# Kernel tuning notes

Measured on AMD Instinct MI355X. Metric: run time of the kernel, lower is better.

The kernel has to match this reference:

```python
import jax, jax.numpy as jnp
import numpy as np

N, H, S = 2048, 512, 256

def setup_inputs() -> dict:
    key = jax.random.key(0)
    k1, k2, k3 = jax.random.split(key, 3)
    hidden_states = jax.random.normal(k1, (N, H, S), dtype=jnp.float32)
    # xavier_uniform-ish scale for W and context vector
    limW = float(np.sqrt(6.0 / (H + H)))
    attention_weights = jax.random.uniform(k2, (H, H), dtype=jnp.float32, minval=-limW, maxval=limW)
    attention_bias = jnp.zeros((H, 1), dtype=jnp.float32)
    limc = float(np.sqrt(6.0 / (H + 1)))
    context_vector = jax.random.uniform(k3, (H, 1), dtype=jnp.float32, minval=-limc, maxval=limc)
    return {
        "hidden_states": hidden_states,
        "attention_weights": attention_weights,
        "attention_bias": attention_bias,
        "context_vector": context_vector,
    }

def reference(hidden_states, attention_weights, attention_bias, context_vector):
    # hidden_states: (N, H, S)
    hs_t = jnp.swapaxes(hidden_states, 1, 2)              # (N, S, H)
    score = jnp.tanh(hs_t @ attention_weights + attention_bias[:, 0])  # (N, S, H)
    alignment = (score @ context_vector)[..., 0]          # (N, S)
    attn = jax.nn.softmax(alignment, axis=1)              # (N, S)
    context = jnp.einsum('ns,nhs->nh', attn, hidden_states)  # (N, H)
    return context
```

## Files before the change

kernel.cpp:

```cpp
#include <hip/hip_runtime.h>
#include <hip/hip_bf16.h>
#include <stdint.h>
#include <stddef.h>

typedef __attribute__((ext_vector_type(8))) short short8;
typedef __attribute__((ext_vector_type(4))) short short4v;
typedef __attribute__((ext_vector_type(4))) float f32x4;
typedef __attribute__((ext_vector_type(16))) float f32x16;

#define NB 2048
#define HD 512
#define SD 256

#define AS_STR 24
#define WS_STR 24

__device__ __forceinline__ short f2bf(float x) {
  __hip_bfloat16 h = __float2bfloat16(x);
  return *reinterpret_cast<short*>(&h);
}

__device__ __forceinline__ float fast_tanh(float x) {
  x = fminf(fmaxf(x, -15.f), 15.f);
  float e = __expf(2.f * x);
  return __fdividef(e - 1.f, e + 1.f);
}

__global__ __launch_bounds__(256) void wconv_kernel(const float* __restrict__ W,
                                                    short* __restrict__ Wtb16) {
  __shared__ float tile[32][33];
  const int bx = blockIdx.x;
  const int tk0 = (bx & 15) * 32;
  const int tj0 = (bx >> 4) * 32;
  const int lx = threadIdx.x & 31;
  const int ly = threadIdx.x >> 5;
  for (int r = 0; r < 4; ++r) {
    int yy = ly + r * 8;
    tile[yy][lx] = W[(size_t)(tk0 + yy) * HD + tj0 + lx];
  }
  __syncthreads();
  for (int r = 0; r < 4; ++r) {
    int yy = ly + r * 8;
    const int k = tk0 + lx;
    Wtb16[(size_t)(k >> 4) * (HD * 16) + (size_t)(tj0 + yy) * 16 + (k & 15)] =
        f2bf(tile[lx][yy]);
  }
}

__global__ void __launch_bounds__(512, 4)
align_kernel(const float* __restrict__ hs, const short* __restrict__ Wtb16,
             const float* __restrict__ bias, const float* __restrict__ ctxv,
             float* __restrict__ align_out)
{
  __shared__ short As[2][64 * AS_STR];
  __shared__ short Ws[2][512 * WS_STR];
  __shared__ float abuf[64];

  const int tid = threadIdx.x;
  const int n = blockIdx.x >> 2;
  const int s0 = (blockIdx.x & 3) * 64;
  const float* hsn = hs + (size_t)n * (HD * SD) + s0;

  if (tid < 64) abuf[tid] = 0.f;

  const int a_s = tid & 63;
  const int a_kq = (tid >> 6) & 3;
  const int w_j = tid;

  if (tid < 256) {
    const float* src = hsn + (size_t)(a_kq * 4) * SD + a_s;
    short4v pk;
    pk[0] = f2bf(src[0]); pk[1] = f2bf(src[SD]);
    pk[2] = f2bf(src[2 * SD]); pk[3] = f2bf(src[3 * SD]);
    *(short4v*)&As[0][a_s * AS_STR + a_kq * 4] = pk;
  }
  {
    const short* wsrc = Wtb16 + (size_t)w_j * 16;
    *(short8*)&Ws[0][w_j * WS_STR] = *(const short8*)wsrc;
    *(short8*)&Ws[0][w_j * WS_STR + 8] = *(const short8*)(wsrc + 8);
  }
  __syncthreads();

  const int lane = tid & 63;
  const int wid = tid >> 6;
  const int jb = wid * 64;
  const int l31 = lane & 31;
  const int hg = lane >> 5;

  f32x16 acc[2][2];
  #pragma unroll
  for (int i = 0; i < 2; ++i)
    #pragma unroll
    for (int p = 0; p < 2; ++p)
      #pragma unroll
      for (int q = 0; q < 16; ++q) acc[i][p][q] = 0.f;

  const int afo = l31 * AS_STR + hg * 8;
  const int wfo = (jb + l31) * WS_STR + hg * 8;

  for (int kt = 0; kt < 32; ++kt) {
    const int cur = kt & 1;

    float av[4];
    short8 wv0, wv1;
    if (kt < 31) {
      if (tid < 256) {
        const float* src = hsn + (size_t)((kt + 1) * 16 + a_kq * 4) * SD + a_s;
        #pragma unroll
        for (int e = 0; e < 4; ++e) av[e] = src[(size_t)e * SD];
      }
      const short* wsrc = Wtb16 + (size_t)(kt + 1) * (HD * 16) + (size_t)w_j * 16;
      wv0 = *(const short8*)wsrc;
      wv1 = *(const short8*)(wsrc + 8);
    }

    short8 wf0 = *(const short8*)&Ws[cur][wfo];
    short8 wf1 = *(const short8*)&Ws[cur][wfo + 32 * WS_STR];
    short8 af0 = *(const short8*)&As[cur][afo];
    short8 af1 = *(const short8*)&As[cur][afo + 32 * AS_STR];

    __builtin_amdgcn_s_setprio(1);
    acc[0][0] = __builtin_amdgcn_mfma_f32_32x32x16_bf16(wf0, af0, acc[0][0], 0, 0, 0);
    acc[0][1] = __builtin_amdgcn_mfma_f32_32x32x16_bf16(wf1, af0, acc[0][1], 0, 0, 0);
    acc[1][0] = __builtin_amdgcn_mfma_f32_32x32x16_bf16(wf0, af1, acc[1][0], 0, 0, 0);
    acc[1][1] = __builtin_amdgcn_mfma_f32_32x32x16_bf16(wf1, af1, acc[1][1], 0, 0, 0);
    __builtin_amdgcn_s_setprio(0);

    if (kt < 31) {
      const int nxt = cur ^ 1;
      if (tid < 256) {
        short4v pk;
        #pragma unroll
        for (int e = 0; e < 4; ++e) pk[e] = f2bf(av[e]);
        *(short4v*)&As[nxt][a_s * AS_STR + a_kq * 4] = pk;
      }
      *(short8*)&Ws[nxt][w_j * WS_STR] = wv0;
      *(short8*)&Ws[nxt][w_j * WS_STR + 8] = wv1;
    }
    __syncthreads();
  }

  float part0 = 0.f, part1 = 0.f;
  #pragma unroll
  for (int p = 0; p < 2; ++p) {
    const int jfr = jb + p * 32 + hg * 4;
    #pragma unroll
    for (int g = 0; g < 4; ++g) {
      const int j4 = jfr + g * 8;
      f32x4 bv = *(const f32x4*)(bias + j4);
      f32x4 cv = *(const f32x4*)(ctxv + j4);
      #pragma unroll
      for (int r = 0; r < 4; ++r) {
        const int q = g * 4 + r;
        part0 += fast_tanh(acc[0][p][q] + bv[r]) * cv[r];
        part1 += fast_tanh(acc[1][p][q] + bv[r]) * cv[r];
      }
    }
  }
  part0 += __shfl_xor(part0, 32);
  part1 += __shfl_xor(part1, 32);
  if (lane < 32) {
    atomicAdd(&abuf[l31], part0);
    atomicAdd(&abuf[32 + l31], part1);
  }
  __syncthreads();
  if (tid < 64) align_out[(size_t)n * SD + s0 + tid] = abuf[tid];
}

__global__ __launch_bounds__(256) void ctx_kernel(const float* __restrict__ hs,
                                                  const float* __restrict__ align_in,
                                                  float* __restrict__ out)
{
  __shared__ __align__(16) float attn_s[256];
  __shared__ float red[8];
  const int n = blockIdx.x;
  const int t = threadIdx.x;
  const int lane = t & 63, wid = t >> 6;

  float a = align_in[(size_t)n * 256 + t];
  float m = a;
  #pragma unroll
  for (int off = 32; off; off >>= 1) m = fmaxf(m, __shfl_xor(m, off));
  if (lane == 0) red[wid] = m;
  __syncthreads();
  m = fmaxf(fmaxf(red[0], red[1]), fmaxf(red[2], red[3]));
  float e = __expf(a - m);
  float s = e;
  #pragma unroll
  for (int off = 32; off; off >>= 1) s += __shfl_xor(s, off);
  if (lane == 0) red[4 + wid] = s;
  __syncthreads();
  s = red[4] + red[5] + red[6] + red[7];
  attn_s[t] = e / s;
  __syncthreads();

  const int grp = t & 7;
  const int hrow = t >> 3;
  float av[32];
  #pragma unroll
  for (int u = 0; u < 8; ++u) {
    float4 v = *(const float4*)&attn_s[grp * 32 + u * 4];
    av[4*u+0] = v.x; av[4*u+1] = v.y; av[4*u+2] = v.z; av[4*u+3] = v.w;
  }
  const float* hb = hs + (size_t)n * (HD * SD) + grp * 32;
  for (int it = 0; it < 16; ++it) {
    const int h = it * 32 + hrow;
    const float4* p = (const float4*)(hb + (size_t)h * SD);
    float acc = 0.f;
    #pragma unroll
    for (int u = 0; u < 8; ++u) {
      float4 v = p[u];
      acc += av[4*u+0]*v.x + av[4*u+1]*v.y + av[4*u+2]*v.z + av[4*u+3]*v.w;
    }
    acc += __shfl_xor(acc, 1);
    acc += __shfl_xor(acc, 2);
    acc += __shfl_xor(acc, 4);
    if (grp == 0) out[(size_t)n * HD + h] = acc;
  }
}

extern "C" void kernel_launch(void* const* d_in, const int* in_sizes, int n_in,
                              void* d_out, int out_size, void* d_ws, size_t ws_size,
                              hipStream_t stream) {
  (void)in_sizes; (void)n_in; (void)out_size; (void)ws_size;
  const float* hs = (const float*)d_in[0];
  const float* W  = (const float*)d_in[1];
  const float* b  = (const float*)d_in[2];
  const float* c  = (const float*)d_in[3];
  float* out = (float*)d_out;

  float* align_ws = (float*)d_ws;
  short* Wtb16 = (short*)((char*)d_ws + (size_t)NB * SD * 4);

  wconv_kernel<<<256, 256, 0, stream>>>(W, Wtb16);
  align_kernel<<<NB * 4, 512, 0, stream>>>(hs, Wtb16, b, c, align_ws);
  ctx_kernel<<<NB, 256, 0, stream>>>(hs, align_ws, out);
}
```

Baseline: 806.3 us.

## Stage full activation tile once in LDS and stream W fragments from global

New measurement: 714.2 us. 1.13x faster.

```diff
diff --git a/kernel.cpp b/kernel.cpp
--- a/kernel.cpp
+++ b/kernel.cpp
@@ -4,7 +4,6 @@
 #include <stddef.h>
 
 typedef __attribute__((ext_vector_type(8))) short short8;
-typedef __attribute__((ext_vector_type(4))) short short4v;
 typedef __attribute__((ext_vector_type(4))) float f32x4;
 typedef __attribute__((ext_vector_type(16))) float f32x16;
 
@@ -12,8 +11,7 @@
 #define HD 512
 #define SD 256
 
-#define AS_STR 24
-#define WS_STR 24
+#define AROW 516
 
 __device__ __forceinline__ short f2bf(float x) {
   __hip_bfloat16 h = __float2bfloat16(x);
@@ -52,8 +50,7 @@
              const float* __restrict__ bias, const float* __restrict__ ctxv,
              float* __restrict__ align_out)
 {
-  __shared__ short As[2][64 * AS_STR];
-  __shared__ short Ws[2][512 * WS_STR];
+  __shared__ short As[64 * AROW];
   __shared__ float abuf[64];
 
   const int tid = threadIdx.x;
@@ -63,21 +60,18 @@
 
   if (tid < 64) abuf[tid] = 0.f;
 
-  const int a_s = tid & 63;
-  const int a_kq = (tid >> 6) & 3;
-  const int w_j = tid;
-
-  if (tid < 256) {
-    const float* src = hsn + (size_t)(a_kq * 4) * SD + a_s;
-    short4v pk;
-    pk[0] = f2bf(src[0]); pk[1] = f2bf(src[SD]);
-    pk[2] = f2bf(src[2 * SD]); pk[3] = f2bf(src[3 * SD]);
-    *(short4v*)&As[0][a_s * AS_STR + a_kq * 4] = pk;
-  }
   {
-    const short* wsrc = Wtb16 + (size_t)w_j * 16;
-    *(short8*)&Ws[0][w_j * WS_STR] = *(const short8*)wsrc;
-    *(short8*)&Ws[0][w_j * WS_STR + 8] = *(const short8*)(wsrc + 8);
+    const int a_s = tid & 63;
+    const int a_kg = tid >> 6;
+    #pragma unroll
+    for (int o = 0; o < 8; ++o) {
+      const int k0 = a_kg * 64 + o * 8;
+      const float* src = hsn + (size_t)k0 * SD + a_s;
+      short8 pk;
+      #pragma unroll
+      for (int e = 0; e < 8; ++e) pk[e] = f2bf(src[(size_t)e * SD]);
+      *(short8*)&As[a_s * AROW + k0] = pk;
+    }
   }
   __syncthreads();
 
@@ -95,29 +89,16 @@
       #pragma unroll
       for (int q = 0; q < 16; ++q) acc[i][p][q] = 0.f;
 
-  const int afo = l31 * AS_STR + hg * 8;
-  const int wfo = (jb + l31) * WS_STR + hg * 8;
-
-  for (int kt = 0; kt < 32; ++kt) {
-    const int cur = kt & 1;
-
-    float av[4];
-    short8 wv0, wv1;
-    if (kt < 31) {
-      if (tid < 256) {
-        const float* src = hsn + (size_t)((kt + 1) * 16 + a_kq * 4) * SD + a_s;
-        #pragma unroll
-        for (int e = 0; e < 4; ++e) av[e] = src[(size_t)e * SD];
-      }
-      const short* wsrc = Wtb16 + (size_t)(kt + 1) * (HD * 16) + (size_t)w_j * 16;
-      wv0 = *(const short8*)wsrc;
-      wv1 = *(const short8*)(wsrc + 8);
-    }
-
-    short8 wf0 = *(const short8*)&Ws[cur][wfo];
-    short8 wf1 = *(const short8*)&Ws[cur][wfo + 32 * WS_STR];
-    short8 af0 = *(const short8*)&As[cur][afo];
-    short8 af1 = *(const short8*)&As[cur][afo + 32 * AS_STR];
+  const short* wlane = Wtb16 + (size_t)(jb + l31) * 16 + hg * 8;
+  const int afo = l31 * AROW + hg * 8;
+
+  #pragma unroll 4
+  for (int kb = 0; kb < 32; ++kb) {
+    const short* wk = wlane + (size_t)kb * (HD * 16);
+    short8 wf0 = *(const short8*)(wk);
+    short8 wf1 = *(const short8*)(wk + 32 * 16);
+    short8 af0 = *(const short8*)&As[afo + kb * 16];
+    short8 af1 = *(const short8*)&As[afo + 32 * AROW + kb * 16];
 
     __builtin_amdgcn_s_setprio(1);
     acc[0][0] = __builtin_amdgcn_mfma_f32_32x32x16_bf16(wf0, af0, acc[0][0], 0, 0, 0);
@@ -125,19 +106,6 @@
     acc[1][0] = __builtin_amdgcn_mfma_f32_32x32x16_bf16(wf0, af1, acc[1][0], 0, 0, 0);
     acc[1][1] = __builtin_amdgcn_mfma_f32_32x32x16_bf16(wf1, af1, acc[1][1], 0, 0, 0);
     __builtin_amdgcn_s_setprio(0);
-
-    if (kt < 31) {
-      const int nxt = cur ^ 1;
-      if (tid < 256) {
-        short4v pk;
-        #pragma unroll
-        for (int e = 0; e < 4; ++e) pk[e] = f2bf(av[e]);
-        *(short4v*)&As[nxt][a_s * AS_STR + a_kq * 4] = pk;
-      }
-      *(short8*)&Ws[nxt][w_j * WS_STR] = wv0;
-      *(short8*)&Ws[nxt][w_j * WS_STR + 8] = wv1;
-    }
-    __syncthreads();
   }
 
   float part0 = 0.f, part1 = 0.f;
```
